# Performance work log

Hardware: AMD Instinct MI355X
Metric: run time of the kernel (lower is better)

The kernel has to match this reference:

```python
import jax, jax.numpy as jnp
import numpy as np

N = 100000      # num_nodes
E = 1600000     # num_edges (avg degree 16)
EMB = 128       # emb_dim
HID = 128       # hidden_size
REPR = 64       # repr_dim


def setup_inputs() -> dict:
    key = jax.random.key(0)
    k0, k1, k2, k3 = jax.random.split(key, 4)
    edge_index = jax.random.randint(k0, (2, E), 0, N)
    node_emb = jax.random.normal(k1, (N, EMB), jnp.float32) * 0.1
    # GCNConv weights: glorot-like init, bias zeros (PyG default)
    W1 = jax.random.normal(k2, (EMB, HID), jnp.float32) * (1.0 / np.sqrt(EMB))
    b1 = jnp.zeros((HID,), jnp.float32)
    W2 = jax.random.normal(k3, (HID, REPR), jnp.float32) * (1.0 / np.sqrt(HID))
    b2 = jnp.zeros((REPR,), jnp.float32)
    return {"edge_index": edge_index, "node_emb": node_emb,
            "W1": W1, "b1": b1, "W2": W2, "b2": b2}


def reference(edge_index, node_emb, W1, b1, W2, b2):
    # PyG GCNConv: add self-loops, symmetric degree normalization,
    # out = scatter_add(norm * (x W)[src] -> dst) + b
    loops = jnp.arange(N, dtype=edge_index.dtype)
    src = jnp.concatenate([edge_index[0], loops])  # [E+N]
    dst = jnp.concatenate([edge_index[1], loops])
    deg = jax.ops.segment_sum(jnp.ones_like(src, dtype=node_emb.dtype), dst,
                              num_segments=N)
    dinv = jax.lax.rsqrt(deg)  # deg >= 1 thanks to self-loops
    norm = dinv[src] * dinv[dst]  # [E+N]

    def gcn_conv(x, W, b):
        h = x @ W                                   # [N, out]
        msg = norm[:, None] * h[src]                # gather + scale, [E+N, out]
        return jax.ops.segment_sum(msg, dst, num_segments=N) + b

    x = jax.nn.relu(gcn_conv(node_emb, W1, b1))
    # F.dropout(training=False) is identity in eval mode
    return gcn_conv(x, W2, b2)
```

## Files before the change

### kernel.cpp

```cpp
#include <hip/hip_runtime.h>
#include <hip/hip_bf16.h>
#include <stdint.h>


static constexpr int KD = 128;
static constexpr int BSH = 8;
static constexpr int MAXB = 512;
static constexpr int CHUNK = 2048;
static constexpr int CAP = 6144;

typedef short bf16x8 __attribute__((ext_vector_type(8)));
typedef float f32x4  __attribute__((ext_vector_type(4)));
typedef float f32x2  __attribute__((ext_vector_type(2)));

__device__ __forceinline__ unsigned short f2bf(float f) {
    __hip_bfloat16 b = __float2bfloat16(f);
    return *reinterpret_cast<unsigned short*>(&b);
}
__device__ __forceinline__ float bflo(unsigned v) { return __uint_as_float(v << 16); }
__device__ __forceinline__ float bfhi(unsigned v) { return __uint_as_float(v & 0xffff0000u); }
__device__ __forceinline__ unsigned pk2(float lo, float hi) {
    return (unsigned)f2bf(lo) | ((unsigned)f2bf(hi) << 16);
}
__device__ __forceinline__ void accp(f32x2* a, uint4 v) {
    f32x2 t;
    t.x = bflo(v.x); t.y = bfhi(v.x); a[0] += t;
    t.x = bflo(v.y); t.y = bfhi(v.y); a[1] += t;
    t.x = bflo(v.z); t.y = bfhi(v.z); a[2] += t;
    t.x = bflo(v.w); t.y = bfhi(v.w); a[3] += t;
}
__device__ __forceinline__ void accf(f32x2* a, uint4 v, float d) {
    f32x2 dd; dd.x = d; dd.y = d;
    f32x2 t;
    t.x = bflo(v.x); t.y = bfhi(v.x); a[0] += dd * t;
    t.x = bflo(v.y); t.y = bfhi(v.y); a[1] += dd * t;
    t.x = bflo(v.z); t.y = bfhi(v.z); a[2] += dd * t;
    t.x = bflo(v.w); t.y = bfhi(v.w); a[3] += dd * t;
}

__global__ __launch_bounds__(256) void init_hist(const float* __restrict__ W1,
        const float* __restrict__ W2, unsigned short* __restrict__ Wt1,
        unsigned short* __restrict__ Wt2, const int* __restrict__ dst,
        int* __restrict__ ghist, int e, int nbuck) {
    __shared__ int cnt[MAXB];
    const int t = threadIdx.x;
    const int e0 = blockIdx.x * CHUNK;
    const int m = min(CHUNK, e - e0);
    for (int i = t; i < nbuck; i += 256) cnt[i] = 0;
    __syncthreads();
    for (int i = t; i < m; i += 256) atomicAdd(&cnt[dst[e0 + i] >> BSH], 1);
    int g = blockIdx.x * 256 + t;
    if (g < 128 * 128) {
        int k = g >> 7, nn = g & 127;
        Wt1[nn * 128 + k] = f2bf(W1[g]);
    } else if (g < 128 * 128 + 128 * 64) {
        int i = g - 128 * 128;
        int k = i >> 6, nn = i & 63;
        Wt2[nn * 128 + k] = f2bf(W2[i]);
    }
    __syncthreads();
    for (int i = t; i < nbuck; i += 256) ghist[blockIdx.x * nbuck + i] = cnt[i];
}

__global__ __launch_bounds__(256) void chunk_scan(int* __restrict__ ghist,
        int* __restrict__ bcur, int nchunk, int nbuck) {
    __shared__ int wsum[4];
    const int t = threadIdx.x;
    const int b = blockIdx.x;
    const int lane = t & 63, wv = t >> 6;
    int carry = 0;
    for (int t0 = 0; t0 < nchunk; t0 += 256) {
        int c = t0 + t;
        int v = (c < nchunk) ? ghist[c * nbuck + b] : 0;
        int iv = v;
        for (int off = 1; off < 64; off <<= 1) {
            int u = __shfl_up(iv, off, 64);
            if (lane >= off) iv += u;
        }
        if (lane == 63) wsum[wv] = iv;
        __syncthreads();
        int woff = 0;
        for (int i = 0; i < wv; ++i) woff += wsum[i];
        int total = wsum[0] + wsum[1] + wsum[2] + wsum[3];
        int excl = iv - v + woff;
        if (c < nchunk) ghist[c * nbuck + b] = b * CAP + carry + excl;
        carry += total;
        __syncthreads();
    }
    if (t == 0) bcur[b] = b * CAP + carry;
}

__global__ __launch_bounds__(256) void scatter_gemm(const int* __restrict__ src,
        const int* __restrict__ dst, const int* __restrict__ ghist,
        int* __restrict__ packed, int e, int nbuck, int nscatter,
        const float* __restrict__ xv, const unsigned short* __restrict__ Wt,
        unsigned short* __restrict__ out, int n)
{
    constexpr int C = 128;
    constexpr int KP = KD + 8;
    constexpr int WP = 64 + 8;
    __shared__ __align__(16) unsigned short xt[64 * KP];
    __shared__ __align__(16) unsigned short lw[C * WP];
    __shared__ int cur[MAXB];
    const int t = threadIdx.x;

    if (blockIdx.x < nscatter) {
        const int e0 = blockIdx.x * CHUNK;
        const int m = min(CHUNK, e - e0);
        for (int i = t; i < nbuck; i += 256) cur[i] = ghist[blockIdx.x * nbuck + i];
        __syncthreads();
        for (int i = t; i < m; i += 256) {
            int d = dst[e0 + i], s = src[e0 + i];
            int b = d >> BSH;
            int p = atomicAdd(&cur[b], 1);
            if (p < (b + 1) * CAP)
                packed[p] = ((d & ((1 << BSH) - 1)) << 24) | s;
        }
        return;
    }

    const int w = t >> 6, lane = t & 63;
    const int quad = lane >> 4, l16 = lane & 15;
    const int row0 = (blockIdx.x - nscatter) * 64;

    for (int i = t; i < 64 * 32; i += 256) {
        int r = i >> 5, c4 = (i & 31) * 4;
        int row = row0 + r;
        ushort4 pk = make_ushort4(0, 0, 0, 0);
        if (row < n) {
            float4 v = *reinterpret_cast<const float4*>(&xv[(size_t)row * KD + c4]);
            pk.x = f2bf(v.x); pk.y = f2bf(v.y); pk.z = f2bf(v.z); pk.w = f2bf(v.w);
        }
        *reinterpret_cast<ushort4*>(&xt[r * KP + c4]) = pk;
    }

    f32x4 acc[C / 16];
#pragma unroll
    for (int i = 0; i < C / 16; ++i) acc[i] = (f32x4)(0.f);

    for (int h = 0; h < 2; ++h) {
        __syncthreads();
        for (int i = t; i < C * 16; i += 256) {
            int nr = i >> 4, j = (i & 15) * 4;
            *reinterpret_cast<ushort4*>(&lw[nr * WP + j]) =
                *reinterpret_cast<const ushort4*>(&Wt[nr * KD + h * 64 + j]);
        }
        __syncthreads();
#pragma unroll
        for (int kt = 0; kt < 2; ++kt) {
            bf16x8 af = *reinterpret_cast<const bf16x8*>(
                &xt[(w * 16 + l16) * KP + h * 64 + kt * 32 + quad * 8]);
#pragma unroll
            for (int ct = 0; ct < C / 16; ++ct) {
                bf16x8 bfr = *reinterpret_cast<const bf16x8*>(
                    &lw[(ct * 16 + l16) * WP + kt * 32 + quad * 8]);
                acc[ct] = __builtin_amdgcn_mfma_f32_16x16x32_bf16(af, bfr, acc[ct], 0, 0, 0);
            }
        }
    }
#pragma unroll
    for (int j = 0; j < 4; ++j) {
        int row = row0 + w * 16 + quad * 4 + j;
        if (row < n) {
#pragma unroll
            for (int ct = 0; ct < C / 16; ++ct)
                out[(size_t)row * C + ct * 16 + l16] = f2bf(acc[ct][j]);
        }
    }
}

__global__ __launch_bounds__(256) void bucket_build(const int* __restrict__ packed,
        const int* __restrict__ bcur, int* __restrict__ roff, int* __restrict__ degN,
        float* __restrict__ dinv, int* __restrict__ csr, int n) {
    __shared__ int deg[1 << BSH];
    __shared__ int cur[1 << BSH];
    __shared__ int wsum[4];
    const int t = threadIdx.x;
    const int b = blockIdx.x;
    const int nodeBase = b << BSH;
    const int nn = min(1 << BSH, n - nodeBase);
    const int e0 = b * CAP, e1 = bcur[b];

    deg[t] = 0;
    __syncthreads();
    for (int i = e0 + t; i < e1; i += 256)
        atomicAdd(&deg[(unsigned)packed[i] >> 24], 1);
    __syncthreads();

    const int d = deg[t];
    int lane = t & 63, wv = t >> 6;
    int iv = d;
    for (int off = 1; off < 64; off <<= 1) {
        int u = __shfl_up(iv, off, 64);
        if (lane >= off) iv += u;
    }
    if (lane == 63) wsum[wv] = iv;
    __syncthreads();
    int woff = 0;
    for (int i = 0; i < wv; ++i) woff += wsum[i];
    int excl = iv - d + woff;
    cur[t] = excl;
    if (t < nn) {
        roff[nodeBase + t] = e0 + excl;
        degN[nodeBase + t] = d;
        dinv[nodeBase + t] = rsqrtf((float)(d + 1));
    }
    __syncthreads();

    for (int i = e0 + t; i < e1; i += 256) {
        unsigned pk = (unsigned)packed[i];
        int dl = pk >> 24;
        int s = pk & 0xFFFFFF;
        int slot = atomicAdd(&cur[dl], 1);
        csr[e0 + slot] = s;
    }
}

__global__ __launch_bounds__(256) void gemm_mfma64(const unsigned short* __restrict__ xv,
        const unsigned short* __restrict__ Wt, const float* __restrict__ dinv,
        unsigned short* __restrict__ out, int n)
{
    constexpr int C = 64;
    constexpr int KP = KD + 8;
    constexpr int WP = 64 + 8;
    __shared__ __align__(16) unsigned short xt[64 * KP];
    __shared__ __align__(16) unsigned short lw[C * WP];
    const int t = threadIdx.x;
    const int w = t >> 6, lane = t & 63;
    const int quad = lane >> 4, l16 = lane & 15;
    const int row0 = blockIdx.x * 64;

    for (int i = t; i < 64 * 32; i += 256) {
        int r = i >> 5, c4 = (i & 31) * 4;
        int row = row0 + r;
        ushort4 pk = make_ushort4(0, 0, 0, 0);
        if (row < n)
            pk = *reinterpret_cast<const ushort4*>(&xv[(size_t)row * KD + c4]);
        *reinterpret_cast<ushort4*>(&xt[r * KP + c4]) = pk;
    }

    f32x4 acc[C / 16];
#pragma unroll
    for (int i = 0; i < C / 16; ++i) acc[i] = (f32x4)(0.f);

    for (int h = 0; h < 2; ++h) {
        __syncthreads();
        for (int i = t; i < C * 16; i += 256) {
            int nr = i >> 4, j = (i & 15) * 4;
            *reinterpret_cast<ushort4*>(&lw[nr * WP + j]) =
                *reinterpret_cast<const ushort4*>(&Wt[nr * KD + h * 64 + j]);
        }
        __syncthreads();
#pragma unroll
        for (int kt = 0; kt < 2; ++kt) {
            bf16x8 af = *reinterpret_cast<const bf16x8*>(
                &xt[(w * 16 + l16) * KP + h * 64 + kt * 32 + quad * 8]);
#pragma unroll
            for (int ct = 0; ct < C / 16; ++ct) {
                bf16x8 bfr = *reinterpret_cast<const bf16x8*>(
                    &lw[(ct * 16 + l16) * WP + kt * 32 + quad * 8]);
                acc[ct] = __builtin_amdgcn_mfma_f32_16x16x32_bf16(af, bfr, acc[ct], 0, 0, 0);
            }
        }
    }
#pragma unroll
    for (int j = 0; j < 4; ++j) {
        int row = row0 + w * 16 + quad * 4 + j;
        if (row < n) {
            float s = dinv[row];
#pragma unroll
            for (int ct = 0; ct < C / 16; ++ct)
                out[(size_t)row * C + ct * 16 + l16] = f2bf(acc[ct][j] * s);
        }
    }
}

__global__ __launch_bounds__(256) void gather128(const uint4* __restrict__ H,
        const int* __restrict__ roff, const int* __restrict__ degN,
        const int* __restrict__ csr, const float* __restrict__ dinv,
        const float* __restrict__ b, uint4* __restrict__ out, int n)
{
    int wid = (blockIdx.x * 256 + threadIdx.x) >> 6;
    int lane = threadIdx.x & 63;
    if (wid >= n) return;
    const int qw = lane >> 4, cp = lane & 15;
    const char* Hb = (const char*)H;
    const unsigned cpo = (unsigned)cp * 16u;
    f32x2 a[4], c[4];
#pragma unroll
    for (int i = 0; i < 4; ++i) { a[i] = (f32x2)(0.f); c[i] = (f32x2)(0.f); }
    int e0 = roff[wid], e1 = e0 + degN[wid];
    for (int base = e0; base < e1; base += 64) {
        int m = e1 - base; if (m > 64) m = 64;
        int idx = (lane < m) ? csr[base + lane] : 0;
        int j = 0;
        for (; j + 8 <= m; j += 8) {
            unsigned u0 = (unsigned)__shfl(idx, j + qw);
            unsigned u1 = (unsigned)__shfl(idx, j + 4 + qw);
            float d0 = dinv[u0], d1 = dinv[u1];
            uint4 v0 = *(const uint4*)(Hb + ((u0 << 8) + cpo));
            uint4 v1 = *(const uint4*)(Hb + ((u1 << 8) + cpo));
            accf(a, v0, d0);
            accf(c, v1, d1);
        }
        for (; j + 4 <= m; j += 4) {
            unsigned u = (unsigned)__shfl(idx, j + qw);
            float d0 = dinv[u];
            uint4 v = *(const uint4*)(Hb + ((u << 8) + cpo));
            accf(a, v, d0);
        }
        int r = m - j;
        if (r) {
            unsigned u = (unsigned)__shfl(idx, min(j + qw, m - 1));
            if (qw < r) {
                float d0 = dinv[u];
                uint4 v = *(const uint4*)(Hb + ((u << 8) + cpo));
                accf(a, v, d0);
            }
        }
    }
#pragma unroll
    for (int i = 0; i < 4; ++i) a[i] += c[i];
#pragma unroll
    for (int i = 0; i < 4; ++i) {
        a[i].x += __shfl_xor(a[i].x, 16, 64);
        a[i].x += __shfl_xor(a[i].x, 32, 64);
        a[i].y += __shfl_xor(a[i].y, 16, 64);
        a[i].y += __shfl_xor(a[i].y, 32, 64);
    }
    if (qw == 0) {
        float s = dinv[wid];
        uint4 sv = *(const uint4*)(Hb + (((unsigned)wid << 8) + cpo));
        accf(a, sv, s);
        float4 b0 = ((const float4*)b)[cp * 2];
        float4 b1 = ((const float4*)b)[cp * 2 + 1];
        float r0 = fmaxf(s * a[0].x + b0.x, 0.f), r1 = fmaxf(s * a[0].y + b0.y, 0.f);
        float r2 = fmaxf(s * a[1].x + b0.z, 0.f), r3 = fmaxf(s * a[1].y + b0.w, 0.f);
        float r4 = fmaxf(s * a[2].x + b1.x, 0.f), r5 = fmaxf(s * a[2].y + b1.y, 0.f);
        float r6 = fmaxf(s * a[3].x + b1.z, 0.f), r7 = fmaxf(s * a[3].y + b1.w, 0.f);
        uint4 o;
        o.x = pk2(r0, r1); o.y = pk2(r2, r3); o.z = pk2(r4, r5); o.w = pk2(r6, r7);
        out[(size_t)wid * 16 + cp] = o;
    }
}

__global__ __launch_bounds__(256) void gather64(const uint4* __restrict__ H,
        const int* __restrict__ roff, const int* __restrict__ degN,
        const int* __restrict__ csr, const float* __restrict__ dinv,
        const float* __restrict__ b, float4* __restrict__ out, int n)
{
    int wquad = (blockIdx.x * 256 + threadIdx.x) >> 6;
    int lane = threadIdx.x & 63;
    const int q16 = lane & 48;
    const int l16 = lane & 15;
    const int oc = l16 >> 3, cp = lane & 7;
    const int node = wquad * 4 + (q16 >> 4);
    const char* Hb = (const char*)H;
    const unsigned cpo = (unsigned)cp * 16u;
    f32x2 a[4], c[4];
#pragma unroll
    for (int i = 0; i < 4; ++i) { a[i] = (f32x2)(0.f); c[i] = (f32x2)(0.f); }
    int e0 = 0, deg = 0;
    if (node < n) { e0 = roff[node]; deg = degN[node]; }
    for (int base = 0; base < deg; base += 16) {
        int m = deg - base; if (m > 16) m = 16;
        int idx = (l16 < m) ? csr[e0 + base + l16] : 0;
        int j = 0;
        for (; j + 4 <= m; j += 4) {
            unsigned u0 = (unsigned)__shfl(idx, q16 + j + oc, 64);
            unsigned u1 = (unsigned)__shfl(idx, q16 + j + 2 + oc, 64);
            uint4 v0 = *(const uint4*)(Hb + ((u0 << 7) + cpo));
            uint4 v1 = *(const uint4*)(Hb + ((u1 << 7) + cpo));
            accp(a, v0);
            accp(c, v1);
        }
        for (; j + 2 <= m; j += 2) {
            unsigned u = (unsigned)__shfl(idx, q16 + j + oc, 64);
            uint4 v = *(const uint4*)(Hb + ((u << 7) + cpo));
            accp(a, v);
        }
        if (j < m) {
            unsigned u = (unsigned)__shfl(idx, q16 + m - 1, 64);
            if (oc == 0) {
                uint4 v = *(const uint4*)(Hb + ((u << 7) + cpo));
                accp(a, v);
            }
        }
    }
#pragma unroll
    for (int i = 0; i < 4; ++i) a[i] += c[i];
#pragma unroll
    for (int i = 0; i < 4; ++i) {
        a[i].x += __shfl_xor(a[i].x, 8, 64);
        a[i].y += __shfl_xor(a[i].y, 8, 64);
    }
    if (oc == 0 && node < n) {
        uint4 sv = *(const uint4*)(Hb + (((unsigned)node << 7) + cpo));
        accp(a, sv);
        float s = dinv[node];
        float4 b0 = ((const float4*)b)[cp * 2];
        float4 b1 = ((const float4*)b)[cp * 2 + 1];
        float4 o0 = make_float4(s * a[0].x + b0.x, s * a[0].y + b0.y,
                                s * a[1].x + b0.z, s * a[1].y + b0.w);
        float4 o1 = make_float4(s * a[2].x + b1.x, s * a[2].y + b1.y,
                                s * a[3].x + b1.z, s * a[3].y + b1.w);
        out[(size_t)node * 16 + cp * 2] = o0;
        out[(size_t)node * 16 + cp * 2 + 1] = o1;
    }
}

extern "C" void kernel_launch(void* const* d_in, const int* in_sizes, int n_in,
                              void* d_out, int out_size, void* d_ws, size_t ws_size,
                              hipStream_t stream)
{
    const int* ei = (const int*)d_in[0];
    const int E = in_sizes[0] / 2;
    const float* emb = (const float*)d_in[1];
    const int N = in_sizes[1] / KD;
    const float* W1 = (const float*)d_in[2];
    const float* b1 = (const float*)d_in[3];
    const float* W2 = (const float*)d_in[4];
    const float* b2 = (const float*)d_in[5];
    const int* src = ei;
    const int* dst = ei + E;
    const int nbuck = (N + (1 << BSH) - 1) >> BSH;
    const int nchunk = (E + CHUNK - 1) / CHUNK;

    char* p = (char*)d_ws;
    auto alloc = [&](size_t bytes) { char* q = p; p += (bytes + 255) & ~(size_t)255; return q; };
    unsigned short* h1 = (unsigned short*)alloc((size_t)N * 128 * sizeof(unsigned short));
    unsigned short* x2 = (unsigned short*)alloc((size_t)N * 128 * sizeof(unsigned short));
    int*   csr    = (int*)  alloc((size_t)nbuck * CAP * sizeof(int));
    int*   packed = (int*)  alloc((size_t)nbuck * CAP * sizeof(int));
    int*   ghist  = (int*)  alloc((size_t)nchunk * nbuck * sizeof(int));
    int*   roff   = (int*)  alloc((size_t)N * sizeof(int));
    int*   degN   = (int*)  alloc((size_t)N * sizeof(int));
    float* dinv   = (float*)alloc((size_t)N * sizeof(float));
    int*   bcur   = (int*)  alloc(MAXB * sizeof(int));
    unsigned short* Wt1 = (unsigned short*)alloc(128 * 128 * sizeof(unsigned short));
    unsigned short* Wt2 = (unsigned short*)alloc(64 * 128 * sizeof(unsigned short));
    unsigned short* h2 = h1;

    init_hist<<<nchunk, 256, 0, stream>>>(W1, W2, Wt1, Wt2, dst, ghist, E, nbuck);
    chunk_scan<<<nbuck, 256, 0, stream>>>(ghist, bcur, nchunk, nbuck);
    const int ngemm1 = (N + 63) / 64;
    scatter_gemm<<<nchunk + ngemm1, 256, 0, stream>>>(src, dst, ghist, packed, E,
                                                      nbuck, nchunk, emb, Wt1, h1, N);
    bucket_build<<<nbuck, 256, 0, stream>>>(packed, bcur, roff, degN, dinv, csr, N);

    gather128<<<(N + 3) / 4, 256, 0, stream>>>((const uint4*)h1, roff, degN, csr,
                                               dinv, b1, (uint4*)x2, N);

    gemm_mfma64<<<(N + 63) / 64, 256, 0, stream>>>(x2, Wt2, dinv, h2, N);
    gather64<<<(N + 15) / 16, 256, 0, stream>>>((const uint4*)h2, roff, degN, csr,
                                                dinv, b2, (float4*)d_out, N);
}
```

Baseline: 280.1 us.

## Split layer-1 gather in halves and overlap second half with layer-2 GEMM

The layer-1 gather now runs in two halves. The second half executes in a combined kernel whose extra blocks run the layer-2 MFMA GEMM on the first half's rows, and a tail GEMM then covers the remaining rows. This means h2 needs its own buffer instead of aliasing h1. Both gather kernels also unroll deeper, with four independent accumulators to keep more loads in flight. The aim is to hide GEMM time under the memory-bound gather and raise memory-level parallelism, at the cost of extra registers and one more launch.

Result: slower. 293.6 us (+4.8%).

```diff
diff --git a/kernel.cpp b/kernel.cpp
--- a/kernel.cpp
+++ b/kernel.cpp
@@ -216,19 +216,95 @@
     }
 }
 
-__global__ __launch_bounds__(256) void gemm_mfma64(const unsigned short* __restrict__ xv,
-        const unsigned short* __restrict__ Wt, const float* __restrict__ dinv,
-        unsigned short* __restrict__ out, int n)
+__device__ __forceinline__ void g128_body(int wid, int lane, const char* Hb,
+        const int* __restrict__ roff, const int* __restrict__ degN,
+        const int* __restrict__ csr, const float* __restrict__ dinv,
+        const float* __restrict__ b, uint4* __restrict__ out)
+{
+    const int qw = lane >> 4, cp = lane & 15;
+    const unsigned cpo = (unsigned)cp * 16u;
+    f32x2 A0[4], A1[4], A2[4], A3[4];
+#pragma unroll
+    for (int i = 0; i < 4; ++i) {
+        A0[i] = (f32x2)(0.f); A1[i] = (f32x2)(0.f);
+        A2[i] = (f32x2)(0.f); A3[i] = (f32x2)(0.f);
+    }
+    int e0 = roff[wid], e1 = e0 + degN[wid];
+    for (int base = e0; base < e1; base += 64) {
+        int m = e1 - base; if (m > 64) m = 64;
+        int idx = (lane < m) ? csr[base + lane] : 0;
+        int j = 0;
+        for (; j + 16 <= m; j += 16) {
+            unsigned u0 = (unsigned)__shfl(idx, j + qw);
+            unsigned u1 = (unsigned)__shfl(idx, j + 4 + qw);
+            unsigned u2 = (unsigned)__shfl(idx, j + 8 + qw);
+            unsigned u3 = (unsigned)__shfl(idx, j + 12 + qw);
+            float d0 = dinv[u0], d1 = dinv[u1], d2 = dinv[u2], d3 = dinv[u3];
+            uint4 v0 = *(const uint4*)(Hb + ((u0 << 8) + cpo));
+            uint4 v1 = *(const uint4*)(Hb + ((u1 << 8) + cpo));
+            uint4 v2 = *(const uint4*)(Hb + ((u2 << 8) + cpo));
+            uint4 v3 = *(const uint4*)(Hb + ((u3 << 8) + cpo));
+            accf(A0, v0, d0); accf(A1, v1, d1); accf(A2, v2, d2); accf(A3, v3, d3);
+        }
+        for (; j + 8 <= m; j += 8) {
+            unsigned u0 = (unsigned)__shfl(idx, j + qw);
+            unsigned u1 = (unsigned)__shfl(idx, j + 4 + qw);
+            float d0 = dinv[u0], d1 = dinv[u1];
+            uint4 v0 = *(const uint4*)(Hb + ((u0 << 8) + cpo));
+            uint4 v1 = *(const uint4*)(Hb + ((u1 << 8) + cpo));
+            accf(A0, v0, d0); accf(A1, v1, d1);
+        }
+        for (; j + 4 <= m; j += 4) {
+            unsigned u = (unsigned)__shfl(idx, j + qw);
+            float d0 = dinv[u];
+            uint4 v = *(const uint4*)(Hb + ((u << 8) + cpo));
+            accf(A0, v, d0);
+        }
+        int r = m - j;
+        if (r) {
+            unsigned u = (unsigned)__shfl(idx, min(j + qw, m - 1));
+            if (qw < r) {
+                float d0 = dinv[u];
+                uint4 v = *(const uint4*)(Hb + ((u << 8) + cpo));
+                accf(A0, v, d0);
+            }
+        }
+    }
+#pragma unroll
+    for (int i = 0; i < 4; ++i) A0[i] = (A0[i] + A1[i]) + (A2[i] + A3[i]);
+#pragma unroll
+    for (int i = 0; i < 4; ++i) {
+        A0[i].x += __shfl_xor(A0[i].x, 16, 64);
+        A0[i].x += __shfl_xor(A0[i].x, 32, 64);
+        A0[i].y += __shfl_xor(A0[i].y, 16, 64);
+        A0[i].y += __shfl_xor(A0[i].y, 32, 64);
+    }
+    if (qw == 0) {
+        float s = dinv[wid];
+        uint4 sv = *(const uint4*)(Hb + (((unsigned)wid << 8) + cpo));
+        accf(A0, sv, s);
+        float4 b0 = ((const float4*)b)[cp * 2];
+        float4 b1 = ((const float4*)b)[cp * 2 + 1];
+        float r0 = fmaxf(s * A0[0].x + b0.x, 0.f), r1 = fmaxf(s * A0[0].y + b0.y, 0.f);
+        float r2 = fmaxf(s * A0[1].x + b0.z, 0.f), r3 = fmaxf(s * A0[1].y + b0.w, 0.f);
+        float r4 = fmaxf(s * A0[2].x + b1.x, 0.f), r5 = fmaxf(s * A0[2].y + b1.y, 0.f);
+        float r6 = fmaxf(s * A0[3].x + b1.z, 0.f), r7 = fmaxf(s * A0[3].y + b1.w, 0.f);
+        uint4 o;
+        o.x = pk2(r0, r1); o.y = pk2(r2, r3); o.z = pk2(r4, r5); o.w = pk2(r6, r7);
+        out[(size_t)wid * 16 + cp] = o;
+    }
+}
+
+__device__ __forceinline__ void gemm64_body(int t, int row0,
+        const unsigned short* __restrict__ xv, const unsigned short* __restrict__ Wt,
+        const float* __restrict__ dinv, unsigned short* __restrict__ out, int n,
+        unsigned short* xt, unsigned short* lw)
 {
     constexpr int C = 64;
     constexpr int KP = KD + 8;
     constexpr int WP = 64 + 8;
-    __shared__ __align__(16) unsigned short xt[64 * KP];
-    __shared__ __align__(16) unsigned short lw[C * WP];
-    const int t = threadIdx.x;
     const int w = t >> 6, lane = t & 63;
     const int quad = lane >> 4, l16 = lane & 15;
-    const int row0 = blockIdx.x * 64;
 
     for (int i = t; i < 64 * 32; i += 256) {
         int r = i >> 5, c4 = (i & 31) * 4;
@@ -278,70 +354,40 @@
 __global__ __launch_bounds__(256) void gather128(const uint4* __restrict__ H,
         const int* __restrict__ roff, const int* __restrict__ degN,
         const int* __restrict__ csr, const float* __restrict__ dinv,
-        const float* __restrict__ b, uint4* __restrict__ out, int n)
-{
-    int wid = (blockIdx.x * 256 + threadIdx.x) >> 6;
-    int lane = threadIdx.x & 63;
-    if (wid >= n) return;
-    const int qw = lane >> 4, cp = lane & 15;
-    const char* Hb = (const char*)H;
-    const unsigned cpo = (unsigned)cp * 16u;
-    f32x2 a[4], c[4];
-#pragma unroll
-    for (int i = 0; i < 4; ++i) { a[i] = (f32x2)(0.f); c[i] = (f32x2)(0.f); }
-    int e0 = roff[wid], e1 = e0 + degN[wid];
-    for (int base = e0; base < e1; base += 64) {
-        int m = e1 - base; if (m > 64) m = 64;
-        int idx = (lane < m) ? csr[base + lane] : 0;
-        int j = 0;
-        for (; j + 8 <= m; j += 8) {
-            unsigned u0 = (unsigned)__shfl(idx, j + qw);
-            unsigned u1 = (unsigned)__shfl(idx, j + 4 + qw);
-            float d0 = dinv[u0], d1 = dinv[u1];
-            uint4 v0 = *(const uint4*)(Hb + ((u0 << 8) + cpo));
-            uint4 v1 = *(const uint4*)(Hb + ((u1 << 8) + cpo));
-            accf(a, v0, d0);
-            accf(c, v1, d1);
-        }
-        for (; j + 4 <= m; j += 4) {
-            unsigned u = (unsigned)__shfl(idx, j + qw);
-            float d0 = dinv[u];
-            uint4 v = *(const uint4*)(Hb + ((u << 8) + cpo));
-            accf(a, v, d0);
-        }
-        int r = m - j;
-        if (r) {
-            unsigned u = (unsigned)__shfl(idx, min(j + qw, m - 1));
-            if (qw < r) {
-                float d0 = dinv[u];
-                uint4 v = *(const uint4*)(Hb + ((u << 8) + cpo));
-                accf(a, v, d0);
-            }
-        }
-    }
-#pragma unroll
-    for (int i = 0; i < 4; ++i) a[i] += c[i];
-#pragma unroll
-    for (int i = 0; i < 4; ++i) {
-        a[i].x += __shfl_xor(a[i].x, 16, 64);
-        a[i].x += __shfl_xor(a[i].x, 32, 64);
-        a[i].y += __shfl_xor(a[i].y, 16, 64);
-        a[i].y += __shfl_xor(a[i].y, 32, 64);
-    }
-    if (qw == 0) {
-        float s = dinv[wid];
-        uint4 sv = *(const uint4*)(Hb + (((unsigned)wid << 8) + cpo));
-        accf(a, sv, s);
-        float4 b0 = ((const float4*)b)[cp * 2];
-        float4 b1 = ((const float4*)b)[cp * 2 + 1];
-        float r0 = fmaxf(s * a[0].x + b0.x, 0.f), r1 = fmaxf(s * a[0].y + b0.y, 0.f);
-        float r2 = fmaxf(s * a[1].x + b0.z, 0.f), r3 = fmaxf(s * a[1].y + b0.w, 0.f);
-        float r4 = fmaxf(s * a[2].x + b1.x, 0.f), r5 = fmaxf(s * a[2].y + b1.y, 0.f);
-        float r6 = fmaxf(s * a[3].x + b1.z, 0.f), r7 = fmaxf(s * a[3].y + b1.w, 0.f);
-        uint4 o;
-        o.x = pk2(r0, r1); o.y = pk2(r2, r3); o.z = pk2(r4, r5); o.w = pk2(r6, r7);
-        out[(size_t)wid * 16 + cp] = o;
-    }
+        const float* __restrict__ b, uint4* __restrict__ out, int n0, int n1)
+{
+    int wid = n0 + ((blockIdx.x * 256 + threadIdx.x) >> 6);
+    if (wid >= n1) return;
+    g128_body(wid, threadIdx.x & 63, (const char*)H, roff, degN, csr, dinv, b, out);
+}
+
+__global__ __launch_bounds__(256) void g128_gemm64(const uint4* __restrict__ H,
+        const int* __restrict__ roff, const int* __restrict__ degN,
+        const int* __restrict__ csr, const float* __restrict__ dinv,
+        const float* __restrict__ b, uint4* __restrict__ out, int half, int n,
+        int nG, const unsigned short* __restrict__ x2,
+        const unsigned short* __restrict__ Wt2, unsigned short* __restrict__ h2)
+{
+    __shared__ __align__(16) unsigned short xt[64 * (KD + 8)];
+    __shared__ __align__(16) unsigned short lw[64 * (64 + 8)];
+    const int t = threadIdx.x;
+    if (blockIdx.x < nG) {
+        int wid = half + ((blockIdx.x * 256 + t) >> 6);
+        if (wid >= n) return;
+        g128_body(wid, t & 63, (const char*)H, roff, degN, csr, dinv, b, out);
+    } else {
+        int row0 = (blockIdx.x - nG) * 64;
+        gemm64_body(t, row0, x2, Wt2, dinv, h2, half, xt, lw);
+    }
+}
+
+__global__ __launch_bounds__(256) void gemm_mfma64(const unsigned short* __restrict__ xv,
+        const unsigned short* __restrict__ Wt, const float* __restrict__ dinv,
+        unsigned short* __restrict__ out, int r0, int n)
+{
+    __shared__ __align__(16) unsigned short xt[64 * (KD + 8)];
+    __shared__ __align__(16) unsigned short lw[64 * (64 + 8)];
+    gemm64_body(threadIdx.x, r0 + blockIdx.x * 64, xv, Wt, dinv, out, n, xt, lw);
 }
 
 __global__ __launch_bounds__(256) void gather64(const uint4* __restrict__ H,
@@ -357,53 +403,66 @@
     const int node = wquad * 4 + (q16 >> 4);
     const char* Hb = (const char*)H;
     const unsigned cpo = (unsigned)cp * 16u;
-    f32x2 a[4], c[4];
-#pragma unroll
-    for (int i = 0; i < 4; ++i) { a[i] = (f32x2)(0.f); c[i] = (f32x2)(0.f); }
+    f32x2 A0[4], A1[4], A2[4], A3[4];
+#pragma unroll
+    for (int i = 0; i < 4; ++i) {
+        A0[i] = (f32x2)(0.f); A1[i] = (f32x2)(0.f);
+        A2[i] = (f32x2)(0.f); A3[i] = (f32x2)(0.f);
+    }
     int e0 = 0, deg = 0;
     if (node < n) { e0 = roff[node]; deg = degN[node]; }
     for (int base = 0; base < deg; base += 16) {
         int m = deg - base; if (m > 16) m = 16;
         int idx = (l16 < m) ? csr[e0 + base + l16] : 0;
         int j = 0;
+        for (; j + 8 <= m; j += 8) {
+            unsigned u0 = (unsigned)__shfl(idx, q16 + j + oc, 64);
+            unsigned u1 = (unsigned)__shfl(idx, q16 + j + 2 + oc, 64);
+            unsigned u2 = (unsigned)__shfl(idx, q16 + j + 4 + oc, 64);
+            unsigned u3 = (unsigned)__shfl(idx, q16 + j + 6 + oc, 64);
+            uint4 v0 = *(const uint4*)(Hb + ((u0 << 7) + cpo));
+            uint4 v1 = *(const uint4*)(Hb + ((u1 << 7) + cpo));
+            uint4 v2 = *(const uint4*)(Hb + ((u2 << 7) + cpo));
+            uint4 v3 = *(const uint4*)(Hb + ((u3 << 7) + cpo));
+            accp(A0, v0); accp(A1, v1); accp(A2, v2); accp(A3, v3);
+        }
         for (; j + 4 <= m; j += 4) {
             unsigned u0 = (unsigned)__shfl(idx, q16 + j + oc, 64);
             unsigned u1 = (unsigned)__shfl(idx, q16 + j + 2 + oc, 64);
             uint4 v0 = *(const uint4*)(Hb + ((u0 << 7) + cpo));
             uint4 v1 = *(const uint4*)(Hb + ((u1 << 7) + cpo));
-            accp(a, v0);
-            accp(c, v1);
+            accp(A0, v0); accp(A1, v1);
         }
         for (; j + 2 <= m; j += 2) {
             unsigned u = (unsigned)__shfl(idx, q16 + j + oc, 64);
             uint4 v = *(const uint4*)(Hb + ((u << 7) + cpo));
-            accp(a, v);
+            accp(A0, v);
         }
         if (j < m) {
             unsigned u = (unsigned)__shfl(idx, q16 + m - 1, 64);
             if (oc == 0) {
                 uint4 v = *(const uint4*)(Hb + ((u << 7) + cpo));
-                accp(a, v);
+                accp(A0, v);
             }
         }
     }
 #pragma unroll
-    for (int i = 0; i < 4; ++i) a[i] += c[i];
+    for (int i = 0; i < 4; ++i) A0[i] = (A0[i] + A1[i]) + (A2[i] + A3[i]);
 #pragma unroll
     for (int i = 0; i < 4; ++i) {
-        a[i].x += __shfl_xor(a[i].x, 8, 64);
-        a[i].y += __shfl_xor(a[i].y, 8, 64);
+        A0[i].x += __shfl_xor(A0[i].x, 8, 64);
+        A0[i].y += __shfl_xor(A0[i].y, 8, 64);
     }
     if (oc == 0 && node < n) {
         uint4 sv = *(const uint4*)(Hb + (((unsigned)node << 7) + cpo));
-        accp(a, sv);
+        accp(A0, sv);
         float s = dinv[node];
         float4 b0 = ((const float4*)b)[cp * 2];
         float4 b1 = ((const float4*)b)[cp * 2 + 1];
-        float4 o0 = make_float4(s * a[0].x + b0.x, s * a[0].y + b0.y,
-                                s * a[1].x + b0.z, s * a[1].y + b0.w);
-        float4 o1 = make_float4(s * a[2].x + b1.x, s * a[2].y + b1.y,
-                                s * a[3].x + b1.z, s * a[3].y + b1.w);
+        float4 o0 = make_float4(s * A0[0].x + b0.x, s * A0[0].y + b0.y,
+                                s * A0[1].x + b0.z, s * A0[1].y + b0.w);
+        float4 o1 = make_float4(s * A0[2].x + b1.x, s * A0[2].y + b1.y,
+                                s * A0[3].x + b1.z, s * A0[3].y + b1.w);
         out[(size_t)node * 16 + cp * 2] = o0;
         out[(size_t)node * 16 + cp * 2 + 1] = o1;
     }
@@ -430,6 +489,7 @@
     auto alloc = [&](size_t bytes) { char* q = p; p += (bytes + 255) & ~(size_t)255; return q; };
     unsigned short* h1 = (unsigned short*)alloc((size_t)N * 128 * sizeof(unsigned short));
     unsigned short* x2 = (unsigned short*)alloc((size_t)N * 128 * sizeof(unsigned short));
+    unsigned short* h2 = (unsigned short*)alloc((size_t)N * 64 * sizeof(unsigned short));
     int*   csr    = (int*)  alloc((size_t)nbuck * CAP * sizeof(int));
     int*   packed = (int*)  alloc((size_t)nbuck * CAP * sizeof(int));
     int*   ghist  = (int*)  alloc((size_t)nchunk * nbuck * sizeof(int));
@@ -439,7 +499,6 @@
     int*   bcur   = (int*)  alloc(MAXB * sizeof(int));
     unsigned short* Wt1 = (unsigned short*)alloc(128 * 128 * sizeof(unsigned short));
     unsigned short* Wt2 = (unsigned short*)alloc(64 * 128 * sizeof(unsigned short));
-    unsigned short* h2 = h1;
 
     init_hist<<<nchunk, 256, 0, stream>>>(W1, W2, Wt1, Wt2, dst, ghist, E, nbuck);
     chunk_scan<<<nbuck, 256, 0, stream>>>(ghist, bcur, nchunk, nbuck);
@@ -448,10 +507,15 @@
                                                       nbuck, nchunk, emb, Wt1, h1, N);
     bucket_build<<<nbuck, 256, 0, stream>>>(packed, bcur, roff, degN, dinv, csr, N);
 
-    gather128<<<(N + 3) / 4, 256, 0, stream>>>((const uint4*)h1, roff, degN, csr,
-                                               dinv, b1, (uint4*)x2, N);
-
-    gemm_mfma64<<<(N + 63) / 64, 256, 0, stream>>>(x2, Wt2, dinv, h2, N);
+    const int half = ((N / 2) + 63) & ~63;
+    gather128<<<half / 4, 256, 0, stream>>>((const uint4*)h1, roff, degN, csr,
+                                            dinv, b1, (uint4*)x2, 0, half);
+    const int nG = (N - half + 3) / 4;
+    g128_gemm64<<<nG + half / 64, 256, 0, stream>>>((const uint4*)h1, roff, degN, csr,
+                                                    dinv, b1, (uint4*)x2, half, N, nG,
+                                                    x2, Wt2, h2);
+    gemm_mfma64<<<(N - half + 63) / 64, 256, 0, stream>>>(x2, Wt2, dinv, h2, half, N);
+
     gather64<<<(N + 15) / 16, 256, 0, stream>>>((const uint4*)h2, roff, degN, csr,
                                                 dinv, b2, (float4*)d_out, N);
 }
```
